# Kernel optimization log

Measured on AMD Instinct MI355X. Metric: run time of the kernel, lower is better.

Reference implementation:

```python
import jax, jax.numpy as jnp
import numpy as np

BS, P, C = 2048, 32, 14

def setup_inputs() -> dict:
    key = jax.random.key(0)
    k1, k2, k3, k4 = jax.random.split(key, 4)
    y_pred = jax.random.uniform(k1, (BS, P, P, C), dtype=jnp.float32)
    eta = jax.random.uniform(k2, (BS, C), dtype=jnp.float32)
    p = jax.random.uniform(k3, (BS, C), dtype=jnp.float32)
    bbox = jax.random.uniform(k4, (BS, C, 4), dtype=jnp.float32)  # normalized x,y,w,h
    return {"y_pred": y_pred, "eta": eta, "p": p, "bbox": bbox}

def reference(y_pred, eta, p, bbox):
    bs = y_pred.shape[0]
    Pdim = y_pred.shape[1]
    yp = jnp.minimum(1.0, y_pred)
    tmp = jnp.minimum(1.0, 1.0 - yp)
    yp = yp * 0.02 + 0.98        # values in [0.98, 1.0]
    tmp = tmp * 0.02 + 0.98
    prod_tmp = jnp.prod(tmp, axis=(1, 2))          # (bs, 14) == p2
    p_y_x = 1.0 - prod_tmp
    # dynamic bbox window -> boolean mask (replaces y_pred[y:y+h, x:x+w] slicing)
    xywh = (bbox * jnp.float32(Pdim)).astype(jnp.int32)  # truncation like K.cast int32
    x0, y0, w, h = xywh[..., 0], xywh[..., 1], xywh[..., 2], xywh[..., 3]
    idx = jnp.arange(Pdim)
    row_m = (idx[None, :, None] >= y0[:, None, :]) & (idx[None, :, None] < (y0 + h)[:, None, :])  # (bs,P,14)
    col_m = (idx[None, :, None] >= x0[:, None, :]) & (idx[None, :, None] < (x0 + w)[:, None, :])  # (bs,P,14)
    mask = row_m[:, :, None, :] & col_m[:, None, :, :]   # (bs,P,P,14)
    p1 = jnp.prod(jnp.where(mask, yp, 1.0), axis=(1, 2))   # prod of y_pred inside bbox
    p3 = jnp.prod(jnp.where(mask, tmp, 1.0), axis=(1, 2))  # prod of tmp inside bbox
    p_y_x_bbox = p1 * prod_tmp / p3 + 1e-10
    loss = (-eta * jnp.log(p_y_x_bbox)
            - (1.0 - eta) * p * jnp.log(p_y_x)
            - (1.0 - eta) * (1.0 - p) * jnp.log(1.0 - p_y_x))
    return jnp.sum(loss) / bs
```

## Files before the change

### kernel.cpp

```cpp
#include <hip/hip_runtime.h>

constexpr int NB = 2048;
constexpr int NP = 32;
constexpr int NC = 14;
constexpr int ELEMS_PER_B = NP * NP * NC;

__global__ __launch_bounds__(448) void loss_main(
    const float* __restrict__ y_pred,
    const float* __restrict__ eta,
    const float* __restrict__ p_in,
    const float* __restrict__ bbox,
    float* __restrict__ partial)
{
    const int b   = blockIdx.x;
    const int tid = threadIdx.x;
    const int c2  = tid % 7;
    const int r   = tid / 7;
    const int j   = r & 31;
    const int rhi = r >> 5;

    __shared__ int   win[NC][4];
    __shared__ float redAll[64][NC];
    __shared__ float red1[64][NC];
    __shared__ float red3[64][NC];
    __shared__ float lossArr[NC];

    if (tid < NC) {
        const float* bb = bbox + ((size_t)b * NC + tid) * 4;
        int x0 = (int)(bb[0] * (float)NP);
        int y0 = (int)(bb[1] * (float)NP);
        int w  = (int)(bb[2] * (float)NP);
        int h  = (int)(bb[3] * (float)NP);
        win[tid][0] = x0;
        win[tid][1] = y0;
        win[tid][2] = x0 + w;
        win[tid][3] = y0 + h;
    }
    __syncthreads();

    const int ca = 2 * c2, cb = ca + 1;
    const int xa0 = win[ca][0], ya0 = win[ca][1], xa1 = win[ca][2], ya1 = win[ca][3];
    const int xb0 = win[cb][0], yb0 = win[cb][1], xb1 = win[cb][2], yb1 = win[cb][3];
    const bool colA = (j >= xa0) && (j < xa1);
    const bool colB = (j >= xb0) && (j < xb1);

    float allA = 1.f, p1A = 1.f, p3A = 1.f;
    float allB = 1.f, p1B = 1.f, p3B = 1.f;

    const float* base = y_pred + (size_t)b * ELEMS_PER_B;

    #pragma unroll
    for (int it = 0; it < 16; ++it) {
        const float2 v = *reinterpret_cast<const float2*>(base + it * 896 + 2 * tid);
        const int i = 2 * it + rhi;
        {
            float yp0 = fminf(1.f, v.x);
            float t0  = fminf(1.f, 1.f - yp0);
            float yp  = fmaf(yp0, 0.02f, 0.98f);
            float t   = fmaf(t0,  0.02f, 0.98f);
            allA *= t;
            bool m = colA && (i >= ya0) && (i < ya1);
            p1A *= m ? yp : 1.f;
            p3A *= m ? t  : 1.f;
        }
        {
            float yp0 = fminf(1.f, v.y);
            float t0  = fminf(1.f, 1.f - yp0);
            float yp  = fmaf(yp0, 0.02f, 0.98f);
            float t   = fmaf(t0,  0.02f, 0.98f);
            allB *= t;
            bool m = colB && (i >= yb0) && (i < yb1);
            p1B *= m ? yp : 1.f;
            p3B *= m ? t  : 1.f;
        }
    }

    redAll[r][ca] = allA;  redAll[r][cb] = allB;
    red1[r][ca]   = p1A;   red1[r][cb]   = p1B;
    red3[r][ca]   = p3A;   red3[r][cb]   = p3B;
    __syncthreads();

    for (int s = 32; s >= 1; s >>= 1) {
        if (tid < s * NC) {
            int rr = tid / NC, cc = tid % NC;
            redAll[rr][cc] *= redAll[rr + s][cc];
            red1[rr][cc]   *= red1[rr + s][cc];
            red3[rr][cc]   *= red3[rr + s][cc];
        }
        __syncthreads();
    }

    if (tid < NC) {
        float Pall = redAll[0][tid];
        float P1   = red1[0][tid];
        float P3   = red3[0][tid];
        float pyx  = 1.f - Pall;
        float pyxb = P1 * Pall / P3 + 1e-10f;
        float e  = eta[(size_t)b * NC + tid];
        float pp = p_in[(size_t)b * NC + tid];
        float loss = -e * logf(pyxb)
                     - (1.f - e) * pp * logf(pyx)
                     - (1.f - e) * (1.f - pp) * logf(Pall);
        lossArr[tid] = loss;
    }
    __syncthreads();

    if (tid == 0) {
        float s = 0.f;
        #pragma unroll
        for (int c = 0; c < NC; ++c) s += lossArr[c];
        partial[b] = s;
    }
}

__global__ __launch_bounds__(256) void reduce_partials(
    const float* __restrict__ partial, float* __restrict__ out)
{
    __shared__ float s[256];
    float acc = 0.f;
    for (int i = threadIdx.x; i < NB; i += 256) acc += partial[i];
    s[threadIdx.x] = acc;
    __syncthreads();
    for (int st = 128; st >= 1; st >>= 1) {
        if (threadIdx.x < st) s[threadIdx.x] += s[threadIdx.x + st];
        __syncthreads();
    }
    if (threadIdx.x == 0) out[0] = s[0] / (float)NB;
}

extern "C" void kernel_launch(void* const* d_in, const int* in_sizes, int n_in,
                              void* d_out, int out_size, void* d_ws, size_t ws_size,
                              hipStream_t stream)
{
    const float* y_pred = (const float*)d_in[0];
    const float* eta    = (const float*)d_in[1];
    const float* p_in   = (const float*)d_in[2];
    const float* bbox   = (const float*)d_in[3];
    float* partial = (float*)d_ws;
    float* out     = (float*)d_out;

    loss_main<<<NB, 448, 0, stream>>>(y_pred, eta, p_in, bbox, partial);
    reduce_partials<<<1, 256, 0, stream>>>(partial, out);
}
```

Measured before the change: 28.59 us.

## Use float4 loads with per-thread 4-element mapping and wider shared reduction

Each thread now loads one float4 per iteration (8 iterations instead of 16 float2 loads), handling four elements that can belong to different channels and row positions. It precomputes channel, column mask and row window per lane. The shared-memory reduction is rebuilt over 128 partial rows per channel, which adds one extra tree step. The final partial-sum kernel now uses 1024 threads with two loads each. The aim is to cut load instruction count and raise memory throughput, at the cost of more registers and a longer shared reduction.

New measurement: 29.64 us. 1.04x slower.

```diff
diff --git a/kernel.cpp b/kernel.cpp
--- a/kernel.cpp
+++ b/kernel.cpp
@@ -4,8 +4,10 @@
 constexpr int NP = 32;
 constexpr int NC = 14;
 constexpr int ELEMS_PER_B = NP * NP * NC;
+constexpr int NT = 448;
+constexpr int NITER = 8;
 
-__global__ __launch_bounds__(448) void loss_main(
+__global__ __launch_bounds__(NT) void loss_main(
     const float* __restrict__ y_pred,
     const float* __restrict__ eta,
     const float* __restrict__ p_in,
@@ -14,15 +16,11 @@
 {
     const int b   = blockIdx.x;
     const int tid = threadIdx.x;
-    const int c2  = tid % 7;
-    const int r   = tid / 7;
-    const int j   = r & 31;
-    const int rhi = r >> 5;
 
     __shared__ int   win[NC][4];
-    __shared__ float redAll[64][NC];
-    __shared__ float red1[64][NC];
-    __shared__ float red3[64][NC];
+    __shared__ float rAll[NC * 128];
+    __shared__ float r1[NC * 128];
+    __shared__ float r3[NC * 128];
     __shared__ float lossArr[NC];
 
     if (tid < NC) {
@@ -38,62 +36,69 @@
     }
     __syncthreads();
 
-    const int ca = 2 * c2, cb = ca + 1;
-    const int xa0 = win[ca][0], ya0 = win[ca][1], xa1 = win[ca][2], ya1 = win[ca][3];
-    const int xb0 = win[cb][0], yb0 = win[cb][1], xb1 = win[cb][2], yb1 = win[cb][3];
-    const bool colA = (j >= xa0) && (j < xa1);
-    const bool colB = (j >= xb0) && (j < xb1);
+    int  ch[4], pB[4], ihi[4], ry0[4], ry1[4];
+    bool col[4];
+    #pragma unroll
+    for (int k = 0; k < 4; ++k) {
+        int f0 = 4 * tid + k;
+        ch[k]  = f0 % NC;
+        pB[k]  = f0 / NC;
+        int j  = pB[k] & 31;
+        ihi[k] = pB[k] >> 5;
+        ry0[k] = win[ch[k]][1];
+        ry1[k] = win[ch[k]][3];
+        col[k] = (j >= win[ch[k]][0]) && (j < win[ch[k]][2]);
+    }
 
-    float allA = 1.f, p1A = 1.f, p3A = 1.f;
-    float allB = 1.f, p1B = 1.f, p3B = 1.f;
+    float aAll[4] = {1.f, 1.f, 1.f, 1.f};
+    float a1[4]   = {1.f, 1.f, 1.f, 1.f};
+    float a3[4]   = {1.f, 1.f, 1.f, 1.f};
 
-    const float* base = y_pred + (size_t)b * ELEMS_PER_B;
+    const float4* base = reinterpret_cast<const float4*>(y_pred + (size_t)b * ELEMS_PER_B);
 
     #pragma unroll
-    for (int it = 0; it < 16; ++it) {
-        const float2 v = *reinterpret_cast<const float2*>(base + it * 896 + 2 * tid);
-        const int i = 2 * it + rhi;
-        {
-            float yp0 = fminf(1.f, v.x);
+    for (int it = 0; it < NITER; ++it) {
+        const float4 v = base[it * NT + tid];
+        const float vv[4] = {v.x, v.y, v.z, v.w};
+        #pragma unroll
+        for (int k = 0; k < 4; ++k) {
+            const int i = 4 * it + ihi[k];
+            float yp0 = fminf(1.f, vv[k]);
             float t0  = fminf(1.f, 1.f - yp0);
             float yp  = fmaf(yp0, 0.02f, 0.98f);
             float t   = fmaf(t0,  0.02f, 0.98f);
-            allA *= t;
-            bool m = colA && (i >= ya0) && (i < ya1);
-            p1A *= m ? yp : 1.f;
-            p3A *= m ? t  : 1.f;
-        }
-        {
-            float yp0 = fminf(1.f, v.y);
-            float t0  = fminf(1.f, 1.f - yp0);
-            float yp  = fmaf(yp0, 0.02f, 0.98f);
-            float t   = fmaf(t0,  0.02f, 0.98f);
-            allB *= t;
-            bool m = colB && (i >= yb0) && (i < yb1);
-            p1B *= m ? yp : 1.f;
-            p3B *= m ? t  : 1.f;
+            aAll[k] *= t;
+            bool m = col[k] && (i >= ry0[k]) && (i < ry1[k]);
+            a1[k] *= m ? yp : 1.f;
+            a3[k] *= m ? t  : 1.f;
         }
     }
 
-    redAll[r][ca] = allA;  redAll[r][cb] = allB;
-    red1[r][ca]   = p1A;   red1[r][cb]   = p1B;
-    red3[r][ca]   = p3A;   red3[r][cb]   = p3B;
+    #pragma unroll
+    for (int k = 0; k < 4; ++k) {
+        const int a = ch[k] * 128 + pB[k];
+        rAll[a] = aAll[k];
+        r1[a]   = a1[k];
+        r3[a]   = a3[k];
+    }
     __syncthreads();
 
-    for (int s = 32; s >= 1; s >>= 1) {
-        if (tid < s * NC) {
-            int rr = tid / NC, cc = tid % NC;
-            redAll[rr][cc] *= redAll[rr + s][cc];
-            red1[rr][cc]   *= red1[rr + s][cc];
-            red3[rr][cc]   *= red3[rr + s][cc];
+    #pragma unroll
+    for (int s = 64; s >= 1; s >>= 1) {
+        for (int idx = tid; idx < NC * s; idx += NT) {
+            const int c = idx / s, m = idx - c * s;
+            const int a = c * 128 + m, a2 = a + s;
+            rAll[a] *= rAll[a2];
+            r1[a]   *= r1[a2];
+            r3[a]   *= r3[a2];
         }
         __syncthreads();
     }
 
     if (tid < NC) {
-        float Pall = redAll[0][tid];
-        float P1   = red1[0][tid];
-        float P3   = red3[0][tid];
+        float Pall = rAll[tid * 128];
+        float P1   = r1[tid * 128];
+        float P3   = r3[tid * 128];
         float pyx  = 1.f - Pall;
         float pyxb = P1 * Pall / P3 + 1e-10f;
         float e  = eta[(size_t)b * NC + tid];
@@ -113,19 +118,18 @@
     }
 }
 
-__global__ __launch_bounds__(256) void reduce_partials(
+__global__ __launch_bounds__(1024) void reduce_partials(
     const float* __restrict__ partial, float* __restrict__ out)
 {
-    __shared__ float s[256];
-    float acc = 0.f;
-    for (int i = threadIdx.x; i < NB; i += 256) acc += partial[i];
-    s[threadIdx.x] = acc;
+    __shared__ float s[1024];
+    const int t = threadIdx.x;
+    s[t] = partial[t] + partial[t + 1024];
     __syncthreads();
-    for (int st = 128; st >= 1; st >>= 1) {
-        if (threadIdx.x < st) s[threadIdx.x] += s[threadIdx.x + st];
+    for (int st = 512; st >= 1; st >>= 1) {
+        if (t < st) s[t] += s[t + st];
         __syncthreads();
     }
-    if (threadIdx.x == 0) out[0] = s[0] / (float)NB;
+    if (t == 0) out[0] = s[0] / (float)NB;
 }
 
 extern "C" void kernel_launch(void* const* d_in, const int* in_sizes, int n_in,
@@ -139,6 +143,6 @@
     float* partial = (float*)d_ws;
     float* out     = (float*)d_out;
 
-    loss_main<<<NB, 448, 0, stream>>>(y_pred, eta, p_in, bbox, partial);
-    reduce_partials<<<1, 256, 0, stream>>>(partial, out);
+    loss_main<<<NB, NT, 0, stream>>>(y_pred, eta, p_in, bbox, partial);
+    reduce_partials<<<1, 1024, 0, stream>>>(partial, out);
 }
```
